# Performance work log

Hardware: AMD Instinct MI355X
Metric: run time of the kernel (lower is better)

## Reference

```python
import jax, jax.numpy as jnp
import numpy as np

EPS = 1e-06
H, D_MODEL = 16, 1024
DK = D_MODEL // H
B, S = 16, 4096


def elu_fea_map(x):
    return jax.nn.elu(x) + 1.0


def setup_inputs() -> dict:
    key = jax.random.key(0)
    ks = jax.random.split(key, 11)
    lim = 1.0 / np.sqrt(D_MODEL)
    u = lambda k, shp: jax.random.uniform(k, shp, jnp.float32, -lim, lim)
    return {
        "query": jax.random.normal(ks[0], (B, D_MODEL), jnp.float32),
        "key": jax.random.normal(ks[1], (B, S, D_MODEL), jnp.float32),
        "value": jax.random.normal(ks[2], (B, S, D_MODEL), jnp.float32),
        "Wq": u(ks[3], (D_MODEL, D_MODEL)), "bq": u(ks[4], (D_MODEL,)),
        "Wk": u(ks[5], (D_MODEL, D_MODEL)), "bk": u(ks[6], (D_MODEL,)),
        "Wv": u(ks[7], (D_MODEL, D_MODEL)), "bv": u(ks[8], (D_MODEL,)),
        "Wo": u(ks[9], (D_MODEL, D_MODEL)), "bo": u(ks[10], (D_MODEL,)),
    }


def reference(query, key, value, Wq, bq, Wk, bk, Wv, bv, Wo, bo):
    nb = query.shape[0]
    # projections; torch Linear: x @ W.T + b
    q = (query @ Wq.T + bq).reshape(nb, 1, H, DK)   # [B,1,H,D]
    k = (key @ Wk.T + bk).reshape(nb, -1, H, DK)    # [B,S,H,D]
    v = (value @ Wv.T + bv).reshape(nb, -1, H, DK)  # [B,S,H,M]
    Q = elu_fea_map(q)
    K = elu_fea_map(k)
    KV = jnp.einsum('bshd,bshm->bhdm', K, v)                      # [B,H,D,M]
    Z = 1.0 / (jnp.einsum('bshd,bhd->bsh', Q, K.sum(axis=1)) + EPS)  # [B,1,H]
    V = jnp.einsum('bshd,bhdm,bsh->bshm', Q, KV, Z)               # [B,1,H,M]
    x = V.reshape(nb, H * DK)
    return x @ Wo.T + bo
```

## Files before the change

kernel.cpp:

```cpp
#include <hip/hip_runtime.h>
#include <hip/hip_bf16.h>
#include <stdint.h>


using bf16 = __hip_bfloat16;
typedef __attribute__((ext_vector_type(8))) short short8;
typedef __attribute__((ext_vector_type(4))) float f32x4;

#define NB_B 16
#define SEQ 4096
#define DM 1024
#define NH 16
#define DKH 64

__device__ __forceinline__ void gload_lds16(const void* g, void* l) {
  __builtin_amdgcn_global_load_lds((const __attribute__((address_space(1))) void*)g,
                                   (__attribute__((address_space(3))) void*)l, 16, 0, 0);
}

__global__ __launch_bounds__(256) void conv_kernel(const float* __restrict__ src,
                                                   bf16* __restrict__ dst, long n4) {
  long i = (long)blockIdx.x * blockDim.x + threadIdx.x;
  const long stride = (long)gridDim.x * blockDim.x;
  for (; i < n4; i += stride) {
    float4 v = ((const float4*)src)[i];
    union { ushort4 u; bf16 h[4]; } o;
    o.h[0] = __float2bfloat16(v.x);
    o.h[1] = __float2bfloat16(v.y);
    o.h[2] = __float2bfloat16(v.z);
    o.h[3] = __float2bfloat16(v.w);
    ((ushort4*)dst)[i] = o.u;
  }
}

template <int KPROJ>
__global__ __launch_bounds__(256) void gemm_proj(
    const float* __restrict__ A, const bf16* __restrict__ W,
    const float* __restrict__ bias, bf16* __restrict__ outT,
    float* __restrict__ Ksum, int rowsTot, int b0, int chunk) {
  __shared__ bf16 As[128 * 64];
  __shared__ bf16 Bs[128 * 64];
  const int tid = threadIdx.x;
  const int lane = tid & 63;
  const int wid = tid >> 6;
  const int wr = wid >> 1, wc = wid & 1;
  const int wgid = (blockIdx.x & 7) * chunk + (blockIdx.x >> 3);
  const int row0 = (wgid >> 3) * 128;
  const int col0 = (wgid & 7) * 128;
  f32x4 acc[4][4] = {};

  char* AsB = (char*)As;
  const int str = tid >> 3;
  const int sslotA = ((tid & 7) ^ (str & 7));
  const int bsrc = (((lane & 7) ^ (lane >> 3)) * 8);
  const int xr = (lane & 7) << 4;
  const int lr = lane & 15;
  const int lk = (lane >> 4) * 16;

  for (int kt = 0; kt < DM / 64; ++kt) {
    const int kb = kt * 64;
#pragma unroll
    for (int i = 0; i < 4; ++i)
      gload_lds16(W + (long)(col0 + wid * 32 + i * 8 + (lane >> 3)) * DM + kb + bsrc,
                  &Bs[(wid * 4 + i) * 512]);
    float4 fa[4][2];
#pragma unroll
    for (int i = 0; i < 4; ++i) {
      const float* src = A + (long)(row0 + i * 32 + str) * DM + kb + (tid & 7) * 8;
      fa[i][0] = *(const float4*)src;
      fa[i][1] = *(const float4*)(src + 4);
    }
#pragma unroll
    for (int i = 0; i < 4; ++i) {
      union { bf16 h[8]; short8 v; } pk;
      pk.h[0] = __float2bfloat16(fa[i][0].x);
      pk.h[1] = __float2bfloat16(fa[i][0].y);
      pk.h[2] = __float2bfloat16(fa[i][0].z);
      pk.h[3] = __float2bfloat16(fa[i][0].w);
      pk.h[4] = __float2bfloat16(fa[i][1].x);
      pk.h[5] = __float2bfloat16(fa[i][1].y);
      pk.h[6] = __float2bfloat16(fa[i][1].z);
      pk.h[7] = __float2bfloat16(fa[i][1].w);
      *(short8*)(AsB + (i * 32 + str) * 128 + (sslotA << 4)) = pk.v;
    }
    __syncthreads();
#pragma unroll
    for (int kk = 0; kk < 2; ++kk) {
      short8 af[4], bfv[4];
#pragma unroll
      for (int m = 0; m < 4; ++m) {
        const int row = wr * 64 + m * 16 + lr;
        af[m] = *(const short8*)(AsB + row * 128 + ((kk * 64 + lk) ^ xr));
      }
#pragma unroll
      for (int n = 0; n < 4; ++n) {
        const int row = wc * 64 + n * 16 + lr;
        bfv[n] = *(const short8*)((char*)Bs + row * 128 + ((kk * 64 + lk) ^ xr));
      }
#pragma unroll
      for (int m = 0; m < 4; ++m)
#pragma unroll
        for (int n = 0; n < 4; ++n)
          acc[m][n] = __builtin_amdgcn_mfma_f32_16x16x32_bf16(af[m], bfv[n], acc[m][n], 0, 0, 0);
    }
    __syncthreads();
  }

  const int bglob = b0 + (row0 >> 12);
#pragma unroll
  for (int n = 0; n < 4; ++n) {
    const int colg = col0 + wc * 64 + n * 16 + (lane & 15);
    const float bv = bias[colg];
    float csum = 0.f;
#pragma unroll
    for (int m = 0; m < 4; ++m) {
      const int r = row0 + wr * 64 + m * 16 + (lane >> 4) * 4;
      union { ushort4 u; bf16 h[4]; } pk;
#pragma unroll
      for (int i = 0; i < 4; ++i) {
        float v = acc[m][n][i] + bv;
        if (KPROJ) { v = v > 0.f ? v + 1.f : __expf(v); csum += v; }
        pk.h[i] = __float2bfloat16(v);
      }
      *(ushort4*)&outT[(long)colg * rowsTot + r] = pk.u;
    }
    if (KPROJ) {
      csum += __shfl_xor(csum, 16);
      csum += __shfl_xor(csum, 32);
      if (lane < 16) atomicAdd(&Ksum[(long)bglob * DM + colg], csum);
    }
  }
}

__global__ __launch_bounds__(256) void kv_kernel(
    const bf16* __restrict__ KT, const bf16* __restrict__ VT,
    float* __restrict__ KVp, int rowsTot, int b0) {
  const int sp = blockIdx.x & 3;
  const int h = (blockIdx.x >> 2) & 15;
  const int b_loc = blockIdx.x >> 6;
  const int lane = threadIdx.x & 63;
  const int w = threadIdx.x >> 6;
  const long srow = (long)b_loc * SEQ + sp * (SEQ / 4) + ((lane >> 4) * 8);
  const bf16* Ab = KT + (long)(h * DKH + w * 16 + (lane & 15)) * rowsTot + srow;
  const bf16* Bb = VT + (long)(h * DKH + (lane & 15)) * rowsTot + srow;
  f32x4 acc[4] = {};
#pragma unroll 2
  for (int s = 0; s < SEQ / 4; s += 32) {
    short8 a = *(const short8*)(Ab + s);
#pragma unroll
    for (int n = 0; n < 4; ++n) {
      short8 bv = *(const short8*)(Bb + (long)n * 16 * rowsTot + s);
      acc[n] = __builtin_amdgcn_mfma_f32_16x16x32_bf16(a, bv, acc[n], 0, 0, 0);
    }
  }
  float* o = KVp + (((long)sp * NB_B + (b0 + b_loc)) * NH + h) * DKH * DKH;
#pragma unroll
  for (int n = 0; n < 4; ++n)
#pragma unroll
    for (int i = 0; i < 4; ++i)
      o[(w * 16 + (lane >> 4) * 4 + i) * DKH + n * 16 + (lane & 15)] = acc[n][i];
}

template <int ELU>
__global__ __launch_bounds__(256) void vecmat_kernel(
    const float* __restrict__ in, const float* __restrict__ W,
    const float* __restrict__ bias, float* __restrict__ outp) {
  const int b = blockIdx.x >> 5;
  const int n0 = (blockIdx.x & 31) * 32;
  const int lane = threadIdx.x & 63;
  const int w = threadIdx.x >> 6;
  float4 qv[4];
#pragma unroll
  for (int it = 0; it < 4; ++it)
    qv[it] = *(const float4*)&in[(long)b * DM + it * 256 + lane * 4];
#pragma unroll
  for (int j = 0; j < 8; ++j) {
    const int n = n0 + w * 8 + j;
    const float* wrow = W + (long)n * DM;
    float s = 0.f;
#pragma unroll
    for (int it = 0; it < 4; ++it) {
      float4 wv = *(const float4*)&wrow[it * 256 + lane * 4];
      s += qv[it].x * wv.x + qv[it].y * wv.y + qv[it].z * wv.z + qv[it].w * wv.w;
    }
    s += __shfl_xor(s, 1);  s += __shfl_xor(s, 2);  s += __shfl_xor(s, 4);
    s += __shfl_xor(s, 8);  s += __shfl_xor(s, 16); s += __shfl_xor(s, 32);
    if (lane == 0) {
      float v = s + bias[n];
      if (ELU) v = v > 0.f ? v + 1.f : __expf(v);
      outp[(long)b * DM + n] = v;
    }
  }
}

__global__ __launch_bounds__(256) void xcomp_kernel(
    const float* __restrict__ Q, const float* __restrict__ KVp,
    const float* __restrict__ Ksum, float* __restrict__ xb) {
  const int b = blockIdx.x;
  const int t = threadIdx.x;
  const int h = t >> 4;
  const int m0 = (t & 15) * 4;
  const float* q = Q + (long)b * DM + h * DKH;
  const float* ks = Ksum + (long)b * DM + h * DKH;
  const long kvoff = ((long)b * NH + h) * DKH * DKH;
  const long spstride = (long)NB_B * NH * DKH * DKH;
  float zden = 0.f;
#pragma unroll
  for (int d = 0; d < DKH; ++d) zden += q[d] * ks[d];
  const float z = 1.f / (zden + 1e-6f);
  float nv[4] = {0.f, 0.f, 0.f, 0.f};
  for (int d = 0; d < DKH; ++d) {
    const float qd = q[d];
#pragma unroll
    for (int j = 0; j < 4; ++j) {
      const long idx = kvoff + d * DKH + m0 + j;
      nv[j] += qd * (KVp[idx] + KVp[idx + spstride] +
                     KVp[idx + 2 * spstride] + KVp[idx + 3 * spstride]);
    }
  }
  float* xo = xb + (long)b * DM + h * DKH + m0;
#pragma unroll
  for (int j = 0; j < 4; ++j) xo[j] = nv[j] * z;
}

extern "C" void kernel_launch(void* const* d_in, const int* in_sizes, int n_in,
                              void* d_out, int out_size, void* d_ws, size_t ws_size,
                              hipStream_t stream) {
  (void)in_sizes; (void)n_in; (void)out_size;
  const float* query = (const float*)d_in[0];
  const float* key   = (const float*)d_in[1];
  const float* value = (const float*)d_in[2];
  const float* Wq = (const float*)d_in[3];
  const float* bq = (const float*)d_in[4];
  const float* Wk = (const float*)d_in[5];
  const float* bk = (const float*)d_in[6];
  const float* Wv = (const float*)d_in[7];
  const float* bv = (const float*)d_in[8];
  const float* Wo = (const float*)d_in[9];
  const float* bo = (const float*)d_in[10];
  float* out = (float*)d_out;

  char* p = (char*)d_ws;
  bf16* WkB = (bf16*)p;  p += (size_t)DM * DM * 2;
  bf16* WvB = (bf16*)p;  p += (size_t)DM * DM * 2;
  float* KVp = (float*)p; p += (size_t)4 * NB_B * NH * DKH * DKH * 4;
  float* Ksum = (float*)p; p += (size_t)NB_B * DM * 4;
  float* Q = (float*)p;  p += (size_t)NB_B * DM * 4;
  float* xb = (float*)p; p += (size_t)NB_B * DM * 4;
  const size_t fixed = (size_t)(p - (char*)d_ws);
  const size_t per_b = (size_t)2 * SEQ * DM * 2;
  if (ws_size < fixed + per_b) return;
  int nbc = (int)((ws_size - fixed) / per_b);
  if (nbc > NB_B) nbc = NB_B;
  bf16* kT = (bf16*)p; p += (size_t)nbc * SEQ * DM * 2;
  bf16* vT = (bf16*)p; p += (size_t)nbc * SEQ * DM * 2;

  hipMemsetAsync(Ksum, 0, (size_t)NB_B * DM * 4, stream);
  conv_kernel<<<512, 256, 0, stream>>>(Wk, WkB, (long)DM * DM / 4);
  conv_kernel<<<512, 256, 0, stream>>>(Wv, WvB, (long)DM * DM / 4);
  vecmat_kernel<1><<<NB_B * 32, 256, 0, stream>>>(query, Wq, bq, Q);

  for (int b0 = 0; b0 < NB_B; b0 += nbc) {
    const int nb = (NB_B - b0 < nbc) ? (NB_B - b0) : nbc;
    const int rows = nb * SEQ;
    const int nwg = (rows / 128) * 8;
    gemm_proj<1><<<nwg, 256, 0, stream>>>(key + (size_t)b0 * SEQ * DM, WkB, bk, kT, Ksum, rows, b0, nwg / 8);
    gemm_proj<0><<<nwg, 256, 0, stream>>>(value + (size_t)b0 * SEQ * DM, WvB, bv, vT, (float*)nullptr, rows, b0, nwg / 8);
    kv_kernel<<<nb * NH * 4, 256, 0, stream>>>(kT, vT, KVp, rows, b0);
  }

  xcomp_kernel<<<NB_B, 256, 0, stream>>>(Q, KVp, Ksum, xb);
  vecmat_kernel<0><<<NB_B * 32, 256, 0, stream>>>(xb, Wo, bo, out);
}
```

Measured before the change: 708.9 us.

## Pre-convert key/value to bf16 and load GEMM A tiles via direct-to-LDS loads

Adds separate conversion passes that turn key and value activations into bf16 buffers, so the projection GEMM can fetch both A and W tiles with asynchronous global-to-LDS loads instead of register loads plus in-kernel conversion. This aims to cut the VGPR pressure and latency of loading A in the GEMM main loop. In exchange it adds an extra full read/write of the large key/value tensors and doubles the workspace needed per batch. The kv kernel loop unroll is also raised.

```diff
diff --git a/kernel.cpp b/kernel.cpp
--- a/kernel.cpp
+++ b/kernel.cpp
@@ -34,8 +34,8 @@
 }
 
 template <int KPROJ>
-__global__ __launch_bounds__(256) void gemm_proj(
-    const float* __restrict__ A, const bf16* __restrict__ W,
+__global__ __launch_bounds__(256) void gemm128(
+    const bf16* __restrict__ A, const bf16* __restrict__ W,
     const float* __restrict__ bias, bf16* __restrict__ outT,
     float* __restrict__ Ksum, int rowsTot, int b0, int chunk) {
   __shared__ bf16 As[128 * 64];
@@ -43,60 +43,43 @@
   const int tid = threadIdx.x;
   const int lane = tid & 63;
   const int wid = tid >> 6;
-  const int wr = wid >> 1, wc = wid & 1;
+  const int wr = wid >> 1;
+  const int wc = wid & 1;
   const int wgid = (blockIdx.x & 7) * chunk + (blockIdx.x >> 3);
   const int row0 = (wgid >> 3) * 128;
   const int col0 = (wgid & 7) * 128;
+
   f32x4 acc[4][4] = {};
 
-  char* AsB = (char*)As;
-  const int str = tid >> 3;
-  const int sslotA = ((tid & 7) ^ (str & 7));
-  const int bsrc = (((lane & 7) ^ (lane >> 3)) * 8);
+  const int lr = lane & 15;
   const int xr = (lane & 7) << 4;
-  const int lr = lane & 15;
   const int lk = (lane >> 4) * 16;
 
-  for (int kt = 0; kt < DM / 64; ++kt) {
+  const bf16* Ab = A + (long)(row0 + wid * 32 + (lane >> 3)) * DM +
+                   ((lane & 7) ^ (lane >> 3)) * 8;
+  const bf16* Wb = W + (long)(col0 + wid * 32 + (lane >> 3)) * DM +
+                   ((lane & 7) ^ (lane >> 3)) * 8;
+
+  for (int kt = 0; kt < 16; ++kt) {
     const int kb = kt * 64;
 #pragma unroll
     for (int i = 0; i < 4; ++i)
-      gload_lds16(W + (long)(col0 + wid * 32 + i * 8 + (lane >> 3)) * DM + kb + bsrc,
-                  &Bs[(wid * 4 + i) * 512]);
-    float4 fa[4][2];
-#pragma unroll
-    for (int i = 0; i < 4; ++i) {
-      const float* src = A + (long)(row0 + i * 32 + str) * DM + kb + (tid & 7) * 8;
-      fa[i][0] = *(const float4*)src;
-      fa[i][1] = *(const float4*)(src + 4);
-    }
-#pragma unroll
-    for (int i = 0; i < 4; ++i) {
-      union { bf16 h[8]; short8 v; } pk;
-      pk.h[0] = __float2bfloat16(fa[i][0].x);
-      pk.h[1] = __float2bfloat16(fa[i][0].y);
-      pk.h[2] = __float2bfloat16(fa[i][0].z);
-      pk.h[3] = __float2bfloat16(fa[i][0].w);
-      pk.h[4] = __float2bfloat16(fa[i][1].x);
-      pk.h[5] = __float2bfloat16(fa[i][1].y);
-      pk.h[6] = __float2bfloat16(fa[i][1].z);
-      pk.h[7] = __float2bfloat16(fa[i][1].w);
-      *(short8*)(AsB + (i * 32 + str) * 128 + (sslotA << 4)) = pk.v;
-    }
+      gload_lds16(Ab + kb + (long)i * 8 * DM, &As[(wid * 4 + i) * 512]);
+#pragma unroll
+    for (int i = 0; i < 4; ++i)
+      gload_lds16(Wb + kb + (long)i * 8 * DM, &Bs[(wid * 4 + i) * 512]);
     __syncthreads();
 #pragma unroll
     for (int kk = 0; kk < 2; ++kk) {
       short8 af[4], bfv[4];
 #pragma unroll
-      for (int m = 0; m < 4; ++m) {
-        const int row = wr * 64 + m * 16 + lr;
-        af[m] = *(const short8*)(AsB + row * 128 + ((kk * 64 + lk) ^ xr));
-      }
-#pragma unroll
-      for (int n = 0; n < 4; ++n) {
-        const int row = wc * 64 + n * 16 + lr;
-        bfv[n] = *(const short8*)((char*)Bs + row * 128 + ((kk * 64 + lk) ^ xr));
-      }
+      for (int m = 0; m < 4; ++m)
+        af[m] = *(const short8*)((char*)As + (wr * 64 + m * 16 + lr) * 128 +
+                                 ((kk * 64 + lk) ^ xr));
+#pragma unroll
+      for (int n = 0; n < 4; ++n)
+        bfv[n] = *(const short8*)((char*)Bs + (wc * 64 + n * 16 + lr) * 128 +
+                                  ((kk * 64 + lk) ^ xr));
 #pragma unroll
       for (int m = 0; m < 4; ++m)
 #pragma unroll
@@ -109,7 +92,7 @@
   const int bglob = b0 + (row0 >> 12);
 #pragma unroll
   for (int n = 0; n < 4; ++n) {
-    const int colg = col0 + wc * 64 + n * 16 + (lane & 15);
+    const int colg = col0 + wc * 64 + n * 16 + lr;
     const float bv = bias[colg];
     float csum = 0.f;
 #pragma unroll
@@ -144,7 +127,7 @@
   const bf16* Ab = KT + (long)(h * DKH + w * 16 + (lane & 15)) * rowsTot + srow;
   const bf16* Bb = VT + (long)(h * DKH + (lane & 15)) * rowsTot + srow;
   f32x4 acc[4] = {};
-#pragma unroll 2
+#pragma unroll 4
   for (int s = 0; s < SEQ / 4; s += 32) {
     short8 a = *(const short8*)(Ab + s);
 #pragma unroll
@@ -248,12 +231,14 @@
   float* Q = (float*)p;  p += (size_t)NB_B * DM * 4;
   float* xb = (float*)p; p += (size_t)NB_B * DM * 4;
   const size_t fixed = (size_t)(p - (char*)d_ws);
-  const size_t per_b = (size_t)2 * SEQ * DM * 2;
+  const size_t per_b = (size_t)4 * SEQ * DM * 2;
   if (ws_size < fixed + per_b) return;
   int nbc = (int)((ws_size - fixed) / per_b);
   if (nbc > NB_B) nbc = NB_B;
-  bf16* kT = (bf16*)p; p += (size_t)nbc * SEQ * DM * 2;
-  bf16* vT = (bf16*)p; p += (size_t)nbc * SEQ * DM * 2;
+  bf16* keyB = (bf16*)p; p += (size_t)nbc * SEQ * DM * 2;
+  bf16* valB = (bf16*)p; p += (size_t)nbc * SEQ * DM * 2;
+  bf16* kT   = (bf16*)p; p += (size_t)nbc * SEQ * DM * 2;
+  bf16* vT   = (bf16*)p; p += (size_t)nbc * SEQ * DM * 2;
 
   hipMemsetAsync(Ksum, 0, (size_t)NB_B * DM * 4, stream);
   conv_kernel<<<512, 256, 0, stream>>>(Wk, WkB, (long)DM * DM / 4);
@@ -263,9 +248,12 @@
   for (int b0 = 0; b0 < NB_B; b0 += nbc) {
     const int nb = (NB_B - b0 < nbc) ? (NB_B - b0) : nbc;
     const int rows = nb * SEQ;
+    const long n4 = (long)rows * DM / 4;
+    conv_kernel<<<2048, 256, 0, stream>>>(key + (size_t)b0 * SEQ * DM, keyB, n4);
+    conv_kernel<<<2048, 256, 0, stream>>>(value + (size_t)b0 * SEQ * DM, valB, n4);
     const int nwg = (rows / 128) * 8;
-    gemm_proj<1><<<nwg, 256, 0, stream>>>(key + (size_t)b0 * SEQ * DM, WkB, bk, kT, Ksum, rows, b0, nwg / 8);
-    gemm_proj<0><<<nwg, 256, 0, stream>>>(value + (size_t)b0 * SEQ * DM, WvB, bv, vT, (float*)nullptr, rows, b0, nwg / 8);
+    gemm128<1><<<nwg, 256, 0, stream>>>(keyB, WkB, bk, kT, Ksum, rows, b0, nwg / 8);
+    gemm128<0><<<nwg, 256, 0, stream>>>(valB, WvB, bv, vT, (float*)nullptr, rows, b0, nwg / 8);
     kv_kernel<<<nb * NH * 4, 256, 0, stream>>>(kT, vT, KVp, rows, b0);
   }
 
```

Result: faster. 660.5 us (-6.8%).
